# Optimization experiments

Measured on AMD Instinct MI355X. Metric: run time of the kernel, lower is better.

Reference implementation:

```python
import jax, jax.numpy as jnp
import numpy as np


def setup_inputs() -> dict:
    key = jax.random.key(0)
    k1, k2 = jax.random.split(key)
    x = jax.random.normal(k1, (128, 25, 512), dtype=jnp.float32)
    high = jax.random.normal(k2, (64, 20, 512), dtype=jnp.float32)  # (C, n, d)
    return {"x": x, "high": high}


def reference(x, high):
    # x: (b, res, d); high: (C, n, d) learned per-class support basis
    b, res, d = x.shape
    C, n, _ = high.shape
    q = x.reshape(b * res, d)                     # (Q, d)
    lam = n / d                                   # ridge coefficient = n/d
    ct = jnp.swapaxes(high, 1, 2)                 # (C, d, n)
    cct = high @ ct                               # (C, n, n) small Gram matrices
    inv = jnp.linalg.inv(cct + lam * jnp.eye(n, dtype=x.dtype))  # (C, n, n)
    ctinv = ct @ inv @ high                       # (C, d, d) per-class projector
    # reconstruct each query through each class projector: (C, Q, d)
    t = jnp.einsum('qd,cde->cqe', q, ctinv)
    dist = jnp.sum((t - q[None, :, :]) ** 2, axis=2).T  # (Q, C)
    logits = -dist.reshape(b, res, C).mean(axis=1)       # (b, C)
    # min-max scaler per row
    mn = logits.min(axis=1, keepdims=True)
    mx = logits.max(axis=1, keepdims=True)
    return (logits - mn) / (mx - mn)
```

## Files before the change

### kernel.cpp

```cpp
#include <hip/hip_runtime.h>

typedef __bf16 v8bf __attribute__((ext_vector_type(8)));
typedef float  v4f  __attribute__((ext_vector_type(4)));

#define D     512
#define NSUP  20
#define NC    64
#define RES   25
#define BB    128
#define LAM   (20.0f/512.0f)
#define KT    32
#define NKT   (D/KT)
#define CPB   8
#define COLS  160
#define NFRAG 10
#define MFRAG 4

__device__ __forceinline__ ushort bf_hi(float v) {
    uint32_t b = __float_as_uint(v);
    return (ushort)((b + 0x7FFF + ((b >> 16) & 1)) >> 16);
}
__device__ __forceinline__ float us2f(ushort u) {
    return __uint_as_float(((uint32_t)u) << 16);
}

__global__ __launch_bounds__(256) void k_prep(const float* __restrict__ high,
                                              ushort* __restrict__ Hth,
                                              ushort* __restrict__ Htl) {
    const int cls = blockIdx.x;
    const int t   = threadIdx.x;
    __shared__ float Hc[NSUP * 516];
    __shared__ float Gs[NSUP * NSUP];
    __shared__ float Lb[NSUP * NSUP];
    __shared__ float Rc[NSUP * NSUP];
    __shared__ float rLb[NSUP];

    for (int i = t; i < NSUP * (D / 4); i += 256) {
        int r = i >> 7, c4 = (i & 127) << 2;
        *(float4*)&Hc[r * 516 + c4] = *(const float4*)&high[(cls * NSUP + r) * D + c4];
    }
    __syncthreads();

    for (int e = t; e < NSUP * NSUP; e += 256) {
        int i = e / NSUP, j = e % NSUP;
        if (i <= j) {
            float s = 0.f;
            for (int k = 0; k < D; k += 4) {
                float4 a = *(float4*)&Hc[i * 516 + k];
                float4 b = *(float4*)&Hc[j * 516 + k];
                s += a.x * b.x + a.y * b.y + a.z * b.z + a.w * b.w;
            }
            Gs[i * NSUP + j] = s;
            Gs[j * NSUP + i] = s;
        }
    }
    __syncthreads();

    if (t < 64) {
        const int c  = t & 31;
        const int gp = t >> 5;
        const float dlam = gp ? 2.0f * LAM : LAM;
        float m[NSUP];
        if (c < NSUP) {
            #pragma unroll
            for (int i = 0; i < NSUP; ++i) m[i] = Gs[i * NSUP + c];
            #pragma unroll
            for (int i = 0; i < NSUP; ++i) if (i == c) m[i] += dlam;
        }
        #pragma unroll
        for (int k = 0; k < NSUP; ++k) {
            float piv = __shfl(m[k], k, 32);
            float sq  = sqrtf(piv);
            float rsq = 1.0f / sq;
            float lck = m[k] * rsq;
            if (c == k) {
                m[k] = sq;
                #pragma unroll
                for (int i = k + 1; i < NSUP; ++i) m[i] *= rsq;
            }
            #pragma unroll
            for (int i = k + 1; i < NSUP; ++i) {
                float lik = __shfl(m[i], k, 32);
                if (c > k) m[i] -= lik * lck;
            }
        }
        if (c < NSUP) {
            float* Lout = gp ? Rc : Lb;
            #pragma unroll
            for (int i = 0; i < NSUP; ++i) {
                if (i > c) Lout[i * NSUP + c] = m[i];
                else if (i == c) {
                    Lout[i * NSUP + c] = m[i];
                    if (!gp) rLb[c] = 1.0f / m[i];
                }
            }
        }
    }
    __syncthreads();

    #pragma unroll
    for (int half = 0; half < 2; ++half) {
        const int col = t + half * 256;
        float h[NSUP];
        #pragma unroll
        for (int m2 = 0; m2 < NSUP; ++m2) h[m2] = Hc[m2 * 516 + col];
        #pragma unroll
        for (int i = 0; i < NSUP; ++i) {
            float s = h[i];
            #pragma unroll
            for (int m2 = 0; m2 < i; ++m2) s -= Lb[i * NSUP + m2] * h[m2];
            h[i] = s * rLb[i];
        }
        #pragma unroll
        for (int i = NSUP - 1; i >= 0; --i) {
            float s = h[i];
            #pragma unroll
            for (int m2 = i + 1; m2 < NSUP; ++m2) s -= Lb[m2 * NSUP + i] * h[m2];
            h[i] = s * rLb[i];
        }
        #pragma unroll
        for (int i = 0; i < NSUP; ++i) {
            float s = 0.f;
            #pragma unroll
            for (int m2 = i; m2 < NSUP; ++m2) s += Rc[m2 * NSUP + i] * h[m2];
            ushort hh = bf_hi(s);
            float  rr = s - us2f(hh);
            Hth[(cls * NSUP + i) * D + col] = hh;
            Htl[(cls * NSUP + i) * D + col] = bf_hi(rr);
        }
    }
}

__global__ __launch_bounds__(256, 2) void k_main(const float* __restrict__ x,
                                                 const ushort* __restrict__ Hth,
                                                 const ushort* __restrict__ Htl,
                                                 float* __restrict__ S) {
    const int cg = blockIdx.x, bp = blockIdx.y;
    const int t = threadIdx.x, lane = t & 63, wid = t >> 6;
    const int wm = wid >> 1, wn = wid & 1;

    __shared__ __align__(16) ushort XH[2][MFRAG * 512];
    __shared__ __align__(16) ushort XL[2][MFRAG * 512];
    __shared__ __align__(16) ushort HH[2][NFRAG * 512];
    __shared__ __align__(16) ushort HL[2][NFRAG * 512];
    __shared__ float colsum[2][COLS];

    v4f acc[2][5];
    #pragma unroll
    for (int a = 0; a < 2; ++a)
        #pragma unroll
        for (int b = 0; b < 5; ++b) acc[a][b] = (v4f){0.f, 0.f, 0.f, 0.f};

    auto stageX = [&](int buf, int kt) {
        #pragma unroll
        for (int s2 = 0; s2 < 2; ++s2) {
            int g = t + 256 * s2;
            int p = g >> 3;
            int k0 = (g & 7) << 2;
            float4 v = make_float4(0.f, 0.f, 0.f, 0.f);
            int r = p & 31;
            if (r < RES)
                v = *(const float4*)&x[(((bp << 1) + (p >> 5)) * RES + r) * D + kt + k0];
            ushort4 hu, lu;
            {
                ushort h; float rr;
                h = bf_hi(v.x); rr = v.x - us2f(h); hu.x = h; lu.x = bf_hi(rr);
                h = bf_hi(v.y); rr = v.y - us2f(h); hu.y = h; lu.y = bf_hi(rr);
                h = bf_hi(v.z); rr = v.z - us2f(h); hu.z = h; lu.z = bf_hi(rr);
                h = bf_hi(v.w); rr = v.w - us2f(h); hu.w = h; lu.w = bf_hi(rr);
            }
            int m = p >> 4, i = p & 15, q = k0 >> 3, off = (k0 & 7);
            int base = m * 512 + (q * 16 + i) * 8 + off;
            *(ushort4*)&XH[buf][base] = hu;
            *(ushort4*)&XL[buf][base] = lu;
        }
    };

    auto stageH = [&](int buf, int kt) {
        #pragma unroll
        for (int j = 0; j < 5; ++j) {
            int cid = wid * 5 + j;
            int n = (cid < 10) ? cid : cid - 10;
            const ushort* src = (cid < 10) ? Hth : Htl;
            ushort* dst = (cid < 10) ? &HH[buf][n * 512] : &HL[buf][n * 512];
            int row = cg * COLS + n * 16 + (lane & 15);
            const ushort* gp = &src[row * D + kt + ((lane >> 4) << 3)];
            __builtin_amdgcn_global_load_lds(
                (const __attribute__((address_space(1))) void*)gp,
                (__attribute__((address_space(3))) void*)dst, 16, 0, 0);
        }
    };

    auto compute = [&](int buf) {
        v8bf ah[2], al[2];
        #pragma unroll
        for (int mf = 0; mf < 2; ++mf) {
            int f = wm * 2 + mf;
            ah[mf] = *(const v8bf*)&XH[buf][f * 512 + lane * 8];
            al[mf] = *(const v8bf*)&XL[buf][f * 512 + lane * 8];
        }
        #pragma unroll
        for (int nf = 0; nf < 5; ++nf) {
            int f = wn * 5 + nf;
            v8bf bh = *(const v8bf*)&HH[buf][f * 512 + lane * 8];
            v8bf bl = *(const v8bf*)&HL[buf][f * 512 + lane * 8];
            #pragma unroll
            for (int mf = 0; mf < 2; ++mf) {
                acc[mf][nf] = __builtin_amdgcn_mfma_f32_16x16x32_bf16(ah[mf], bh, acc[mf][nf], 0, 0, 0);
                acc[mf][nf] = __builtin_amdgcn_mfma_f32_16x16x32_bf16(ah[mf], bl, acc[mf][nf], 0, 0, 0);
                acc[mf][nf] = __builtin_amdgcn_mfma_f32_16x16x32_bf16(al[mf], bh, acc[mf][nf], 0, 0, 0);
                acc[mf][nf] = __builtin_amdgcn_mfma_f32_16x16x32_bf16(al[mf], bl, acc[mf][nf], 0, 0, 0);
            }
        }
    };

    stageX(0, 0);
    stageH(0, 0);
    __syncthreads();
    for (int step = 0; step < NKT; ++step) {
        int cur = step & 1;
        if (step + 1 < NKT) {
            stageH(cur ^ 1, (step + 1) * KT);
            stageX(cur ^ 1, (step + 1) * KT);
        }
        compute(cur);
        __syncthreads();
    }

    #pragma unroll
    for (int nf = 0; nf < 5; ++nf) {
        float part = 0.f;
        #pragma unroll
        for (int mf = 0; mf < 2; ++mf)
            #pragma unroll
            for (int j = 0; j < 4; ++j) part += acc[mf][nf][j] * acc[mf][nf][j];
        part += __shfl_xor(part, 16);
        part += __shfl_xor(part, 32);
        if ((lane >> 4) == 0) colsum[wm][wn * 80 + nf * 16 + lane] = part;
    }
    __syncthreads();
    if (t < 16) {
        int b = t >> 3, c = t & 7;
        float s = 0.f;
        #pragma unroll
        for (int i = 0; i < NSUP; ++i) s += colsum[b][c * 20 + i];
        S[((bp << 1) + b) * NC + cg * CPB + c] = s;
    }
}

__global__ __launch_bounds__(64) void k_minmax(const float* __restrict__ S,
                                               float* __restrict__ out) {
    const int b    = blockIdx.x;
    const int lane = threadIdx.x;
    float s  = S[b * NC + lane];
    float mn = s, mx = s;
    #pragma unroll
    for (int off = 32; off > 0; off >>= 1) {
        mn = fminf(mn, __shfl_xor(mn, off, 64));
        mx = fmaxf(mx, __shfl_xor(mx, off, 64));
    }
    out[b * NC + lane] = (s - mn) / (mx - mn);
}

extern "C" void kernel_launch(void* const* d_in, const int* in_sizes, int n_in,
                              void* d_out, int out_size, void* d_ws, size_t ws_size,
                              hipStream_t stream) {
    const float* x    = (const float*)d_in[0];
    const float* high = (const float*)d_in[1];
    float* out = (float*)d_out;

    ushort* Hth = (ushort*)d_ws;
    ushort* Htl = Hth + NC * NSUP * D;
    float*  S   = (float*)(Htl + NC * NSUP * D);

    k_prep  <<<NC, 256, 0, stream>>>(high, Hth, Htl);
    k_main  <<<dim3(CPB, BB / 2), 256, 0, stream>>>(x, Hth, Htl, S);
    k_minmax<<<BB, 64, 0, stream>>>(S, out);
}
```

Before: 115.0 us.

## Split prep kernel into factorization and solve stages, drop lo*lo MFMA term

The per-class prep kernel is split in two. The first kernel computes the Cholesky factors and reciprocal diagonals and writes them to workspace. The second kernel runs the triangular solves over a (class, column-half) grid, so 128 blocks work on that stage instead of 64. The main GEMM also drops the low×low bf16 split product, which removes a quarter of the MFMAs at the cost of a small accuracy loss and one extra kernel launch.

```diff
diff --git a/kernel.cpp b/kernel.cpp
--- a/kernel.cpp
+++ b/kernel.cpp
@@ -15,6 +15,7 @@
 #define COLS  160
 #define NFRAG 10
 #define MFRAG 4
+#define LRSZ  820
 
 __device__ __forceinline__ ushort bf_hi(float v) {
     uint32_t b = __float_as_uint(v);
@@ -24,16 +25,12 @@
     return __uint_as_float(((uint32_t)u) << 16);
 }
 
-__global__ __launch_bounds__(256) void k_prep(const float* __restrict__ high,
-                                              ushort* __restrict__ Hth,
-                                              ushort* __restrict__ Htl) {
+__global__ __launch_bounds__(256) void k_prep1(const float* __restrict__ high,
+                                               float* __restrict__ LR) {
     const int cls = blockIdx.x;
     const int t   = threadIdx.x;
     __shared__ float Hc[NSUP * 516];
     __shared__ float Gs[NSUP * NSUP];
-    __shared__ float Lb[NSUP * NSUP];
-    __shared__ float Rc[NSUP * NSUP];
-    __shared__ float rLb[NSUP];
 
     for (int i = t; i < NSUP * (D / 4); i += 256) {
         int r = i >> 7, c4 = (i & 127) << 2;
@@ -85,49 +82,54 @@
             }
         }
         if (c < NSUP) {
-            float* Lout = gp ? Rc : Lb;
-            #pragma unroll
-            for (int i = 0; i < NSUP; ++i) {
-                if (i > c) Lout[i * NSUP + c] = m[i];
-                else if (i == c) {
-                    Lout[i * NSUP + c] = m[i];
-                    if (!gp) rLb[c] = 1.0f / m[i];
-                }
-            }
-        }
-    }
-    __syncthreads();
-
-    #pragma unroll
-    for (int half = 0; half < 2; ++half) {
-        const int col = t + half * 256;
-        float h[NSUP];
-        #pragma unroll
-        for (int m2 = 0; m2 < NSUP; ++m2) h[m2] = Hc[m2 * 516 + col];
-        #pragma unroll
-        for (int i = 0; i < NSUP; ++i) {
-            float s = h[i];
-            #pragma unroll
-            for (int m2 = 0; m2 < i; ++m2) s -= Lb[i * NSUP + m2] * h[m2];
-            h[i] = s * rLb[i];
-        }
-        #pragma unroll
-        for (int i = NSUP - 1; i >= 0; --i) {
-            float s = h[i];
-            #pragma unroll
-            for (int m2 = i + 1; m2 < NSUP; ++m2) s -= Lb[m2 * NSUP + i] * h[m2];
-            h[i] = s * rLb[i];
-        }
-        #pragma unroll
-        for (int i = 0; i < NSUP; ++i) {
-            float s = 0.f;
-            #pragma unroll
-            for (int m2 = i; m2 < NSUP; ++m2) s += Rc[m2 * NSUP + i] * h[m2];
-            ushort hh = bf_hi(s);
-            float  rr = s - us2f(hh);
-            Hth[(cls * NSUP + i) * D + col] = hh;
-            Htl[(cls * NSUP + i) * D + col] = bf_hi(rr);
-        }
+            float* base = LR + cls * LRSZ + (gp ? 400 : 0);
+            #pragma unroll
+            for (int i = 0; i < NSUP; ++i) if (i >= c) base[i * NSUP + c] = m[i];
+            if (!gp) LR[cls * LRSZ + 800 + c] = 1.0f / m[c];
+        }
+    }
+}
+
+__global__ __launch_bounds__(256) void k_prep2(const float* __restrict__ high,
+                                               const float* __restrict__ LR,
+                                               ushort* __restrict__ Hth,
+                                               ushort* __restrict__ Htl) {
+    const int cls = blockIdx.x;
+    const int col = blockIdx.y * 256 + threadIdx.x;
+    const int t   = threadIdx.x;
+    __shared__ float Ls[400], Rs[400], rL[NSUP];
+
+    for (int i = t; i < 400; i += 256) Ls[i] = LR[cls * LRSZ + i];
+    for (int i = t; i < 400; i += 256) Rs[i] = LR[cls * LRSZ + 400 + i];
+    if (t < NSUP) rL[t] = LR[cls * LRSZ + 800 + t];
+    __syncthreads();
+
+    float h[NSUP];
+    #pragma unroll
+    for (int m = 0; m < NSUP; ++m) h[m] = high[(cls * NSUP + m) * D + col];
+    #pragma unroll
+    for (int i = 0; i < NSUP; ++i) {
+        float s = h[i];
+        #pragma unroll
+        for (int m = 0; m < i; ++m) s -= Ls[i * NSUP + m] * h[m];
+        h[i] = s * rL[i];
+    }
+    #pragma unroll
+    for (int i = NSUP - 1; i >= 0; --i) {
+        float s = h[i];
+        #pragma unroll
+        for (int m = i + 1; m < NSUP; ++m) s -= Ls[m * NSUP + i] * h[m];
+        h[i] = s * rL[i];
+    }
+    #pragma unroll
+    for (int i = 0; i < NSUP; ++i) {
+        float s = 0.f;
+        #pragma unroll
+        for (int m = i; m < NSUP; ++m) s += Rs[m * NSUP + i] * h[m];
+        ushort hh = bf_hi(s);
+        float  rr = s - us2f(hh);
+        Hth[(cls * NSUP + i) * D + col] = hh;
+        Htl[(cls * NSUP + i) * D + col] = bf_hi(rr);
     }
 }
 
@@ -209,7 +211,6 @@
                 acc[mf][nf] = __builtin_amdgcn_mfma_f32_16x16x32_bf16(ah[mf], bh, acc[mf][nf], 0, 0, 0);
                 acc[mf][nf] = __builtin_amdgcn_mfma_f32_16x16x32_bf16(ah[mf], bl, acc[mf][nf], 0, 0, 0);
                 acc[mf][nf] = __builtin_amdgcn_mfma_f32_16x16x32_bf16(al[mf], bh, acc[mf][nf], 0, 0, 0);
-                acc[mf][nf] = __builtin_amdgcn_mfma_f32_16x16x32_bf16(al[mf], bl, acc[mf][nf], 0, 0, 0);
             }
         }
     };
@@ -272,8 +273,10 @@
     ushort* Hth = (ushort*)d_ws;
     ushort* Htl = Hth + NC * NSUP * D;
     float*  S   = (float*)(Htl + NC * NSUP * D);
-
-    k_prep  <<<NC, 256, 0, stream>>>(high, Hth, Htl);
+    float*  LR  = S + BB * NC;
+
+    k_prep1 <<<NC, 256, 0, stream>>>(high, LR);
+    k_prep2 <<<dim3(NC, 2), 256, 0, stream>>>(high, LR, Hth, Htl);
     k_main  <<<dim3(CPB, BB / 2), 256, 0, stream>>>(x, Hth, Htl, S);
     k_minmax<<<BB, 64, 0, stream>>>(S, out);
 }
```

Result: faster. 110.9 us (-3.6%).
